# Kernel tuning notes

Measured on AMD Instinct MI355X. Metric: run time of the kernel, lower is better.

Reference implementation:

```python
import jax, jax.numpy as jnp
import numpy as np

G, S, D, H, E = 8, 2048, 1024, 4096, 8  # groups, group_size, d_model, ffn_hidden, experts


def setup_inputs() -> dict:
    key = jax.random.key(0)
    ks = jax.random.split(key, 6)
    s = 0.02
    return {
        "x": jax.random.normal(ks[0], (G, S, D), dtype=jnp.float32),
        "gate_w": jax.random.normal(ks[1], (D, E), dtype=jnp.float32) * s,
        "ew1": jax.random.normal(ks[2], (E, D, H), dtype=jnp.float32) * s,
        "eb1": jnp.zeros((E, H), dtype=jnp.float32),
        "ew2": jax.random.normal(ks[3], (E, H, D), dtype=jnp.float32) * s,
        "eb2": jnp.zeros((E, D), dtype=jnp.float32),
        "sw1": jax.random.normal(ks[4], (D, H), dtype=jnp.float32) * s,
        "sb1": jnp.zeros((H,), dtype=jnp.float32),
        "sw2": jax.random.normal(ks[5], (H, D), dtype=jnp.float32) * s,
        "sb2": jnp.zeros((D,), dtype=jnp.float32),
        "expert_capacity": 2048,
    }


def reference(x, gate_w, ew1, eb1, ew2, eb2, sw1, sb1, sw2, sb2, expert_capacity):
    g, s_, d = x.shape
    e = gate_w.shape[1]
    T = g * s_
    cap = int(expert_capacity)

    # ---- Router (inference path) ----
    router_logits = jnp.einsum('gsd,de->gse', x, gate_w)           # (G,S,E)
    router_probs = jax.nn.softmax(router_logits, axis=-1)
    flat_probs = router_probs.transpose(2, 0, 1).reshape(e, T)      # (E,T)
    pad_w = max(0, cap - T)
    if pad_w > 0:
        flat_probs = jnp.pad(flat_probs, ((0, 0), (0, pad_w)),
                             mode='constant', constant_values=-1e9)
    scores, token_indices = jax.lax.top_k(flat_probs, k=cap)        # (E,C)
    scores = jnp.where(scores > -1e8, scores, 0.0)

    # ---- Routed experts: gather -> grouped FFN -> scale -> scatter-add ----
    x_flat = x.reshape(T, d)                                        # (T,D)
    safe_idx = jnp.clip(token_indices, 0, T - 1)                    # guard padded slots
    toks = x_flat[safe_idx]                                         # (E,C,D)
    h = jax.nn.gelu(jnp.einsum('ecd,edh->ech', toks, ew1) + eb1[:, None, :])
    y = jnp.einsum('ech,ehd->ecd', h, ew2) + eb2[:, None, :]        # (E,C,D)
    y = y * scores[..., None]                                       # zero weight kills padded slots
    routed = jnp.zeros_like(x_flat).at[safe_idx.reshape(-1)].add(y.reshape(-1, d))

    # ---- Shared expert over all tokens ----
    shared = jax.nn.gelu(x_flat @ sw1 + sb1) @ sw2 + sb2            # (T,D)

    return (routed + shared).reshape(g, s_, d)
```

## Files before the change

kernel.cpp:

```cpp
#include <hip/hip_runtime.h>

typedef __bf16 bf16;
typedef __bf16 bf16x8 __attribute__((ext_vector_type(8)));
typedef float f32x4 __attribute__((ext_vector_type(4)));

#define NTOK 16384
#define DMODEL 1024
#define HFFN 4096
#define NEXP 8
#define CAP 2048

#define VMCNT(n) asm volatile("s_waitcnt vmcnt(" #n ")" ::: "memory")
#define LGKM0() do { asm volatile("s_waitcnt lgkmcnt(0)" ::: "memory"); \
                     __builtin_amdgcn_sched_barrier(0); } while (0)
#define BARRIER() __builtin_amdgcn_s_barrier()
#define PRIO1() __builtin_amdgcn_s_setprio(1)
#define PRIO0() __builtin_amdgcn_s_setprio(0)

__device__ __forceinline__ void gload16(const void* g, void* l) {
  __builtin_amdgcn_global_load_lds((const __attribute__((address_space(1))) void*)g,
                                   (__attribute__((address_space(3))) void*)l, 16, 0, 0);
}

__device__ __forceinline__ float gelu_f(float v) {
  float t = v * v;
  float s2 = v * fmaf(0.10294358f, t, 2.3022084f);
  float e = __builtin_exp2f(-s2);
  return v * __builtin_amdgcn_rcpf(1.0f + e);
}

__device__ __forceinline__ void xcd_remap(int& bx, int& by) {
  const int gx = gridDim.x;
  const int lg = 31 - __clz((unsigned)gx);
  const int w = blockIdx.x + gx * blockIdx.y;
  bx = (w >> 3) & (gx - 1);
  by = (w & 7) | (((w >> 3) >> lg) << 3);
}

__global__ __launch_bounds__(256) void cvt_x_kernel(const float* __restrict__ x,
                                                    bf16* __restrict__ xb) {
  int i = blockIdx.x * blockDim.x + threadIdx.x;
  const float4* a = (const float4*)x + (size_t)i * 2;
  float4 v0 = a[0], v1 = a[1];
  bf16x8 o;
  o[0]=(bf16)v0.x; o[1]=(bf16)v0.y; o[2]=(bf16)v0.z; o[3]=(bf16)v0.w;
  o[4]=(bf16)v1.x; o[5]=(bf16)v1.y; o[6]=(bf16)v1.z; o[7]=(bf16)v1.w;
  *(bf16x8*)(xb + (size_t)i * 8) = o;
}

__global__ __launch_bounds__(64) void router_kernel(const float* __restrict__ x,
                                                    const float* __restrict__ gw,
                                                    float* __restrict__ probs) {
  int t = blockIdx.x;
  int l = threadIdx.x;
  int e = l & 7, chunk = l >> 3;
  const float* xr = x + (size_t)t * DMODEL + chunk * 128;
  const float* gwr = gw + (size_t)(chunk * 128) * NEXP + e;
  float a0 = 0.f, a1 = 0.f;
  #pragma unroll
  for (int d = 0; d < 128; d += 8) {
    float4 xv = *(const float4*)(xr + d);
    float4 xw = *(const float4*)(xr + d + 4);
    a0 += xv.x * gwr[(d+0)*8] + xv.y * gwr[(d+1)*8] + xv.z * gwr[(d+2)*8] + xv.w * gwr[(d+3)*8];
    a1 += xw.x * gwr[(d+4)*8] + xw.y * gwr[(d+5)*8] + xw.z * gwr[(d+6)*8] + xw.w * gwr[(d+7)*8];
  }
  float acc = a0 + a1;
  acc += __shfl_xor(acc, 8);
  acc += __shfl_xor(acc, 16);
  acc += __shfl_xor(acc, 32);
  float m = acc;
  m = fmaxf(m, __shfl_xor(m, 1));
  m = fmaxf(m, __shfl_xor(m, 2));
  m = fmaxf(m, __shfl_xor(m, 4));
  float ex = expf(acc - m);
  float s = ex;
  s += __shfl_xor(s, 1); s += __shfl_xor(s, 2); s += __shfl_xor(s, 4);
  if (l < 8) probs[(size_t)e * NTOK + t] = ex / s;
}

__global__ __launch_bounds__(256) void topk_kernel(const float* __restrict__ probs,
                                                   int* __restrict__ oidx,
                                                   float* __restrict__ oscr) {
  const int e = blockIdx.x;
  const float* p = probs + (size_t)e * NTOK;
  const int t = threadIdx.x;
  __shared__ unsigned hist[256];
  __shared__ unsigned sg[256], sq[256];
  __shared__ unsigned bcast[4];
  unsigned pref = 0, krem = CAP;
  for (int pass = 0; pass < 4; ++pass) {
    const int sh = 24 - pass * 8;
    hist[t] = 0;
    __syncthreads();
    for (int j = 0; j < 64; ++j) {
      unsigned u = __float_as_uint(p[t * 64 + j]);
      bool ok = (pass == 0) || ((u >> (sh + 8)) == pref);
      if (ok) atomicAdd(&hist[(u >> sh) & 255u], 1u);
    }
    __syncthreads();
    if (t == 0) {
      unsigned cum = 0; int b = 255;
      for (; b > 0; --b) {
        unsigned c = hist[b];
        if (cum + c >= krem) break;
        cum += c;
      }
      bcast[0] = (pref << 8) | (unsigned)b;
      bcast[1] = krem - cum;
    }
    __syncthreads();
    pref = bcast[0];
    krem = bcast[1];
  }
  const unsigned thr = pref;
  const unsigned neq_take = krem;
  unsigned cgt = 0, ceq = 0;
  for (int j = 0; j < 64; ++j) {
    unsigned u = __float_as_uint(p[t * 64 + j]);
    cgt += (u > thr);
    ceq += (u == thr);
  }
  sg[t] = cgt; sq[t] = ceq;
  __syncthreads();
  if (t == 0) {
    unsigned ag = 0, aq = 0;
    for (int i = 0; i < 256; ++i) {
      unsigned g = sg[i], q = sq[i];
      sg[i] = ag; sq[i] = aq;
      ag += g; aq += q;
    }
    bcast[2] = ag;
  }
  __syncthreads();
  const unsigned ngt = bcast[2];
  unsigned og = sg[t], oq = sq[t];
  int* oi = oidx + e * CAP;
  float* os = oscr + e * CAP;
  for (int j = 0; j < 64; ++j) {
    int tok = t * 64 + j;
    float pv = p[tok];
    unsigned u = __float_as_uint(pv);
    if (u > thr) {
      oi[og] = tok; os[og] = pv; ++og;
    } else if (u == thr) {
      if (oq < neq_take) { oi[ngt + oq] = tok; os[ngt + oq] = pv; }
      ++oq;
    }
  }
}

__global__ __launch_bounds__(256) void transpose_cvt(const float* __restrict__ in_e,
                                                     const float* __restrict__ in_s,
                                                     bf16* __restrict__ outp,
                                                     int R, int C) {
  int z = blockIdx.z;
  const float* in = (z < 8) ? (in_e + (size_t)z * (size_t)R * C) : in_s;
  bf16* out = outp + (size_t)z * (size_t)R * C;
  __shared__ float tile[64][65];
  int tx = threadIdx.x & 63, ty = threadIdx.x >> 6;
  int c0 = blockIdx.x * 64, r0 = blockIdx.y * 64;
  #pragma unroll
  for (int j = 0; j < 16; ++j) {
    int r = ty + j * 4;
    tile[r][tx] = in[(size_t)(r0 + r) * C + c0 + tx];
  }
  __syncthreads();
  #pragma unroll
  for (int j = 0; j < 16; ++j) {
    int c = ty + j * 4;
    out[(size_t)(c0 + c) * R + r0 + tx] = (bf16)tile[tx][c];
  }
}


#define STG_ALO(D, ko) { gload16(srcA0 + (ko), (D) + tid8); gload16(srcA2 + (ko), (D) + 4096 + tid8); }
#define STG_AHI(D, ko) { gload16(srcA1 + (ko), (D) + 8192 + tid8); gload16(srcA3 + (ko), (D) + 12288 + tid8); }
#define STG_BLO(D, ko) { gload16(srcBlo0 + (ko), (D) + 16384 + tid8); gload16(srcBlo1 + (ko), (D) + 20480 + tid8); }
#define STG_BHI(D, ko) { gload16(srcBhi0 + (ko), (D) + 24576 + tid8); gload16(srcBhi1 + (ko), (D) + 28672 + tid8); }

#define RD_A(ARR, D, OFF) \
  _Pragma("unroll") for (int i = 0; i < 4; ++i) { \
    ARR[2*i]   = *(const bf16x8*)((D) + (OFF) + (wr*64 + i*16 + fr)*64 + c0s); \
    ARR[2*i+1] = *(const bf16x8*)((D) + (OFF) + (wr*64 + i*16 + fr)*64 + c1s); \
  }
#define RD_B(ARR, D, OFF) \
  _Pragma("unroll") for (int j = 0; j < 2; ++j) { \
    ARR[2*j]   = *(const bf16x8*)((D) + (OFF) + (wc*32 + j*16 + fr)*64 + c0s); \
    ARR[2*j+1] = *(const bf16x8*)((D) + (OFF) + (wc*32 + j*16 + fr)*64 + c1s); \
  }

#define MFMA_Q(I0, J0, A, B) \
  _Pragma("unroll") for (int i = 0; i < 4; ++i) \
    _Pragma("unroll") for (int j = 0; j < 2; ++j) { \
      acc[(I0)+i][(J0)+j] = __builtin_amdgcn_mfma_f32_16x16x32_bf16((A)[2*i],   (B)[2*j],   acc[(I0)+i][(J0)+j], 0, 0, 0); \
      acc[(I0)+i][(J0)+j] = __builtin_amdgcn_mfma_f32_16x16x32_bf16((A)[2*i+1], (B)[2*j+1], acc[(I0)+i][(J0)+j], 0, 0, 0); \
    }

#define KLOOP(NT) do { \
  bf16* B0_ = smem; \
  bf16* B1_ = smem + 32768; \
   \
  STG_ALO(B0_, 0); STG_BLO(B0_, 0); STG_BHI(B0_, 0); STG_AHI(B0_, 0); \
  STG_ALO(B1_, 64); STG_BLO(B1_, 64); STG_BHI(B1_, 64); \
  VMCNT(6); \
  BARRIER(); \
  RD_A(aA, B0_, 0); RD_B(aB, B0_, 16384); \
  for (int t = 0; t < (NT); t += 2) { \
    const bool st = (t + 2) < (NT); \
    const int ko1 = (t + 1) * 64, ko2 = (t + 2) * 64, ko3 = (t + 3) * 64; \
     \
    LGKM0(); \
    STG_AHI(B1_, ko1); \
    PRIO1(); MFMA_Q(0, 0, aA, aB); PRIO0(); \
    if (st) { VMCNT(10); } else { VMCNT(0); } \
    RD_B(bB, B0_, 24576); \
    BARRIER(); \
     \
    LGKM0(); \
    if (st) STG_ALO(B0_, ko2); \
    PRIO1(); MFMA_Q(0, 2, aA, bB); PRIO0(); \
    if (st) { VMCNT(10); } else { VMCNT(0); } \
    RD_A(aA, B0_, 8192); \
    BARRIER(); \
     \
    LGKM0(); \
    if (st) STG_BLO(B0_, ko2); \
    PRIO1(); MFMA_Q(4, 2, aA, bB); PRIO0(); \
    BARRIER(); \
     \
    LGKM0(); \
    if (st) STG_BHI(B0_, ko2); \
    PRIO1(); MFMA_Q(4, 0, aA, aB); PRIO0(); \
    if (st) { VMCNT(8); } else { VMCNT(0); } \
    RD_A(aA, B1_, 0); RD_B(aB, B1_, 16384); \
    BARRIER(); \
     \
    LGKM0(); \
    if (st) STG_AHI(B0_, ko2); \
    PRIO1(); MFMA_Q(0, 0, aA, aB); PRIO0(); \
    RD_B(bB, B1_, 24576); \
    BARRIER(); \
     \
    LGKM0(); \
    if (st) STG_ALO(B1_, ko3); \
    PRIO1(); MFMA_Q(0, 2, aA, bB); PRIO0(); \
    if (st) { VMCNT(10); } else { VMCNT(0); } \
    RD_A(aA, B1_, 8192); \
    BARRIER(); \
     \
    LGKM0(); \
    if (st) STG_BLO(B1_, ko3); \
    PRIO1(); MFMA_Q(4, 2, aA, bB); PRIO0(); \
    BARRIER(); \
     \
    LGKM0(); \
    if (st) STG_BHI(B1_, ko3); \
    PRIO1(); MFMA_Q(4, 0, aA, aB); PRIO0(); \
    if (st) { VMCNT(10); } else { VMCNT(0); } \
    if (st) { RD_A(aA, B0_, 0); RD_B(aB, B0_, 16384); } \
    BARRIER(); \
  } \
} while (0)

__global__ __launch_bounds__(512, 2) void ffn1_gemm(const bf16* __restrict__ xb,
                                                    const bf16* __restrict__ w1t,
                                                    const float* __restrict__ bias1,
                                                    const int* __restrict__ sel,
                                                    bf16* __restrict__ hout,
                                                    int routed) {
  const int e = blockIdx.z;
  const bf16* Bw = w1t + (routed ? (size_t)e * HFFN * DMODEL : 0);
  const float* bias = bias1 + (routed ? (size_t)e * HFFN : 0);
  bf16* hb = hout + (routed ? (size_t)e * CAP * HFFN : 0);
  int bx, by;
  xcd_remap(bx, by);
  const int m0 = by * 256, n0 = bx * 256;
  __shared__ __align__(16) bf16 smem[65536];
  const int tid = threadIdx.x, lane = tid & 63, wave = tid >> 6;
  const int wr = wave >> 2, wc = wave & 3;
  const int tid8 = tid * 8;

  const int p = tid >> 3, sch = tid & 7;
  const int schs = sch ^ (p & 7);
  const int brow = p + (p & 32);
  const bf16 *srcA0, *srcA1, *srcA2, *srcA3, *srcBlo0, *srcBlo1, *srcBhi0, *srcBhi1;
  {
    int ra0 = routed ? sel[e * CAP + m0 + p]       : (m0 + p);
    int ra1 = routed ? sel[e * CAP + m0 + 64 + p]  : (m0 + 64 + p);
    int ra2 = routed ? sel[e * CAP + m0 + 128 + p] : (m0 + 128 + p);
    int ra3 = routed ? sel[e * CAP + m0 + 192 + p] : (m0 + 192 + p);
    srcA0 = xb + (size_t)ra0 * DMODEL + schs * 8;
    srcA1 = xb + (size_t)ra1 * DMODEL + schs * 8;
    srcA2 = xb + (size_t)ra2 * DMODEL + schs * 8;
    srcA3 = xb + (size_t)ra3 * DMODEL + schs * 8;
    srcBlo0 = Bw + (size_t)(n0 + brow) * DMODEL + schs * 8;
    srcBlo1 = srcBlo0 + (size_t)128 * DMODEL;
    srcBhi0 = srcBlo0 + (size_t)32 * DMODEL;
    srcBhi1 = srcBlo0 + (size_t)160 * DMODEL;
  }

  f32x4 acc[8][4];
  #pragma unroll
  for (int i = 0; i < 8; ++i)
    #pragma unroll
    for (int j = 0; j < 4; ++j) acc[i][j] = (f32x4){0.f, 0.f, 0.f, 0.f};

  const int fr = lane & 15;
  const int k8 = lane >> 4;
  const int sw = lane & 7;
  const int c0s = (k8 ^ sw) * 8;
  const int c1s = ((k8 + 4) ^ sw) * 8;
  bf16x8 aA[8], aB[4], bB[4];

  KLOOP(DMODEL / 64);

  __syncthreads();
  #pragma unroll
  for (int half = 0; half < 2; ++half) {
    if (wr == half) {
      #pragma unroll
      for (int i = 0; i < 8; ++i) {
        #pragma unroll
        for (int j = 0; j < 4; ++j) {
          const int nl = wc * 64 + j * 16 + fr;
          const float bb = bias[n0 + nl];
          #pragma unroll
          for (int q = 0; q < 4; ++q) {
            const int ml = i * 16 + (lane >> 4) * 4 + q;
            smem[ml * 256 + (nl ^ (((ml >> 2) & 7) << 4))] =
                (bf16)gelu_f(acc[i][j][q] + bb);
          }
        }
      }
    }
    __syncthreads();
    #pragma unroll
    for (int pp = 0; pp < 8; ++pp) {
      const int flat = pp * 512 + tid;
      const int row = flat >> 5, nc8 = flat & 31;
      uint4 v = *(const uint4*)(smem + row * 256 + ((nc8 * 8) ^ (((row >> 2) & 7) << 4)));
      *(uint4*)(hb + (size_t)(m0 + half * 128 + row) * HFFN + n0 + nc8 * 8) = v;
    }
    __syncthreads();
  }
}

__global__ __launch_bounds__(512, 2) void ffn2_gemm(const bf16* __restrict__ hbuf,
                                                    const bf16* __restrict__ w2t,
                                                    const float* __restrict__ bias2,
                                                    const int* __restrict__ sel,
                                                    const float* __restrict__ scr,
                                                    float* __restrict__ out,
                                                    int routed) {
  const int e = blockIdx.z;
  const bf16* Ab = hbuf + (routed ? (size_t)e * CAP * HFFN : 0);
  const bf16* Bw = w2t + (routed ? (size_t)e * DMODEL * HFFN : 0);
  const float* bias = bias2 + (routed ? (size_t)e * DMODEL : 0);
  int bx, by;
  xcd_remap(bx, by);
  const int m0 = by * 256, n0 = bx * 256;
  __shared__ __align__(16) bf16 smem[65536];
  __shared__ int s_tok[256];
  __shared__ float s_scl[256];
  const int tid = threadIdx.x, lane = tid & 63, wave = tid >> 6;
  const int wr = wave >> 2, wc = wave & 3;
  const int tid8 = tid * 8;

  const int p = tid >> 3, sch = tid & 7;
  const int schs = sch ^ (p & 7);
  const int brow = p + (p & 32);
  const bf16* srcA0 = Ab + (size_t)(m0 + p) * HFFN + schs * 8;
  const bf16* srcA1 = Ab + (size_t)(m0 + 64 + p) * HFFN + schs * 8;
  const bf16* srcA2 = Ab + (size_t)(m0 + 128 + p) * HFFN + schs * 8;
  const bf16* srcA3 = Ab + (size_t)(m0 + 192 + p) * HFFN + schs * 8;
  const bf16* srcBlo0 = Bw + (size_t)(n0 + brow) * HFFN + schs * 8;
  const bf16* srcBlo1 = srcBlo0 + (size_t)128 * HFFN;
  const bf16* srcBhi0 = srcBlo0 + (size_t)32 * HFFN;
  const bf16* srcBhi1 = srcBlo0 + (size_t)160 * HFFN;
  if (routed && tid < 256) {
    s_tok[tid] = sel[e * CAP + m0 + tid];
    s_scl[tid] = scr[e * CAP + m0 + tid];
  }

  f32x4 acc[8][4];
  #pragma unroll
  for (int i = 0; i < 8; ++i)
    #pragma unroll
    for (int j = 0; j < 4; ++j) acc[i][j] = (f32x4){0.f, 0.f, 0.f, 0.f};

  const int fr = lane & 15;
  const int k8 = lane >> 4;
  const int sw = lane & 7;
  const int c0s = (k8 ^ sw) * 8;
  const int c1s = ((k8 + 4) ^ sw) * 8;
  bf16x8 aA[8], aB[4], bB[4];

  KLOOP(HFFN / 64);

  if (!routed) {
    #pragma unroll
    for (int i = 0; i < 8; ++i) {
      #pragma unroll
      for (int j = 0; j < 4; ++j) {
        const int nl = wc * 64 + j * 16 + fr;
        const float bb = bias[n0 + nl];
        #pragma unroll
        for (int q = 0; q < 4; ++q) {
          const int ml = wr * 128 + i * 16 + (lane >> 4) * 4 + q;
          out[(size_t)(m0 + ml) * DMODEL + n0 + nl] = acc[i][j][q] + bb;
        }
      }
    }
  } else {
    __syncthreads();
    #pragma unroll
    for (int i = 0; i < 8; ++i) {
      #pragma unroll
      for (int j = 0; j < 4; ++j) {
        const int nl = wc * 64 + j * 16 + fr;
        const float bb = bias[n0 + nl];
        #pragma unroll
        for (int q = 0; q < 4; ++q) {
          const int ml = wr * 128 + i * 16 + (lane >> 4) * 4 + q;
          const int tok = s_tok[ml];
          const float sc = s_scl[ml];
          atomicAdd(out + (size_t)tok * DMODEL + n0 + nl, (acc[i][j][q] + bb) * sc);
        }
      }
    }
  }
}

extern "C" void kernel_launch(void* const* d_in, const int* in_sizes, int n_in,
                              void* d_out, int out_size, void* d_ws, size_t ws_size,
                              hipStream_t stream) {
  const float* x   = (const float*)d_in[0];
  const float* gw  = (const float*)d_in[1];
  const float* ew1 = (const float*)d_in[2];
  const float* eb1 = (const float*)d_in[3];
  const float* ew2 = (const float*)d_in[4];
  const float* eb2 = (const float*)d_in[5];
  const float* sw1 = (const float*)d_in[6];
  const float* sb1 = (const float*)d_in[7];
  const float* sw2 = (const float*)d_in[8];
  const float* sb2 = (const float*)d_in[9];
  float* out = (float*)d_out;

  char* ws = (char*)d_ws;
  size_t off = 0;
  bf16* xb      = (bf16*)(ws + off); off += (size_t)NTOK * DMODEL * 2;
  bf16* w1t     = (bf16*)(ws + off); off += (size_t)9 * HFFN * DMODEL * 2;
  bf16* w2t     = (bf16*)(ws + off); off += (size_t)9 * DMODEL * HFFN * 2;
  bf16* hbuf    = (bf16*)(ws + off); off += (size_t)NTOK * HFFN * 2;
  float* probs  = (float*)(ws + off); off += (size_t)NEXP * NTOK * 4;
  int* selidx   = (int*)(ws + off);   off += (size_t)NEXP * CAP * 4;
  float* selscr = (float*)(ws + off); off += (size_t)NEXP * CAP * 4;

  cvt_x_kernel<<<dim3(NTOK * DMODEL / 8 / 256), dim3(256), 0, stream>>>(x, xb);
  router_kernel<<<dim3(NTOK), dim3(64), 0, stream>>>(x, gw, probs);
  topk_kernel<<<dim3(NEXP), dim3(256), 0, stream>>>(probs, selidx, selscr);
  transpose_cvt<<<dim3(HFFN / 64, DMODEL / 64, 9), dim3(256), 0, stream>>>(ew1, sw1, w1t, DMODEL, HFFN);
  transpose_cvt<<<dim3(DMODEL / 64, HFFN / 64, 9), dim3(256), 0, stream>>>(ew2, sw2, w2t, HFFN, DMODEL);

  ffn1_gemm<<<dim3(HFFN / 256, NTOK / 256, 1), dim3(512), 0, stream>>>(
      xb, w1t + (size_t)8 * HFFN * DMODEL, sb1, (const int*)nullptr, hbuf, 0);
  ffn2_gemm<<<dim3(DMODEL / 256, NTOK / 256, 1), dim3(512), 0, stream>>>(
      hbuf, w2t + (size_t)8 * DMODEL * HFFN, sb2, (const int*)nullptr, (const float*)nullptr, out, 0);

  ffn1_gemm<<<dim3(HFFN / 256, CAP / 256, NEXP), dim3(512), 0, stream>>>(
      xb, w1t, eb1, selidx, hbuf, 1);
  ffn2_gemm<<<dim3(DMODEL / 256, CAP / 256, NEXP), dim3(512), 0, stream>>>(
      hbuf, w2t, eb2, selidx, selscr, out, 1);
}
```

Measured before the change: 838.3 us.

## Reschedule GEMM K-loop with two barriers per phase and rotating B fragment registers

Restructures the ping-pong LDS pipeline in the shared KLOOP macro used by both FFN GEMMs. Each MFMA quarter is now bracketed by a barrier before and after, with the LDS fragment reads issued just ahead of it. The B fragments rotate between two register sets (S1/S2), and the prologue now waits for the whole first stage to land instead of a partial vmcnt. The aim is to tighten the order of LDS reads against global-to-LDS staging and keep waves in lockstep. In exchange it doubles the barrier count and may expose more LDS latency before each MFMA group.

```diff
diff --git a/kernel.cpp b/kernel.cpp
--- a/kernel.cpp
+++ b/kernel.cpp
@@ -199,65 +199,61 @@
 #define KLOOP(NT) do { \
   bf16* B0_ = smem; \
   bf16* B1_ = smem + 32768; \
-   \
-  STG_ALO(B0_, 0); STG_BLO(B0_, 0); STG_BHI(B0_, 0); STG_AHI(B0_, 0); \
-  STG_ALO(B1_, 64); STG_BLO(B1_, 64); STG_BHI(B1_, 64); \
-  VMCNT(6); \
+  STG_ALO(B0_, 0); STG_BHI(B0_, 0); STG_AHI(B0_, 0); STG_BLO(B0_, 0); \
+  VMCNT(0); \
   BARRIER(); \
-  RD_A(aA, B0_, 0); RD_B(aB, B0_, 16384); \
+  RD_B(S1, B0_, 16384); \
+  STG_BLO(B1_, 64); STG_ALO(B1_, 64); STG_BHI(B1_, 64); \
   for (int t = 0; t < (NT); t += 2) { \
     const bool st = (t + 2) < (NT); \
-    const int ko1 = (t + 1) * 64, ko2 = (t + 2) * 64, ko3 = (t + 3) * 64; \
-     \
-    LGKM0(); \
+    const int ko1 = (t+1)*64, ko2 = (t+2)*64, ko3 = (t+3)*64; \
+     \
+    RD_A(aA, B0_, 0); \
     STG_AHI(B1_, ko1); \
-    PRIO1(); MFMA_Q(0, 0, aA, aB); PRIO0(); \
-    if (st) { VMCNT(10); } else { VMCNT(0); } \
-    RD_B(bB, B0_, 24576); \
-    BARRIER(); \
-     \
-    LGKM0(); \
+    BARRIER(); LGKM0(); \
+    PRIO1(); MFMA_Q(0,0,aA,S1); PRIO0(); \
+    BARRIER(); \
+     \
+    RD_B(S2, B0_, 24576); \
+    if (st) STG_BLO(B0_, ko2); \
+    BARRIER(); LGKM0(); \
+    PRIO1(); MFMA_Q(0,2,aA,S2); PRIO0(); \
+    BARRIER(); \
+     \
+    RD_A(aA, B0_, 8192); \
     if (st) STG_ALO(B0_, ko2); \
-    PRIO1(); MFMA_Q(0, 2, aA, bB); PRIO0(); \
-    if (st) { VMCNT(10); } else { VMCNT(0); } \
-    RD_A(aA, B0_, 8192); \
-    BARRIER(); \
-     \
-    LGKM0(); \
-    if (st) STG_BLO(B0_, ko2); \
-    PRIO1(); MFMA_Q(4, 2, aA, bB); PRIO0(); \
-    BARRIER(); \
-     \
-    LGKM0(); \
-    if (st) STG_BHI(B0_, ko2); \
-    PRIO1(); MFMA_Q(4, 0, aA, aB); PRIO0(); \
-    if (st) { VMCNT(8); } else { VMCNT(0); } \
-    RD_A(aA, B1_, 0); RD_B(aB, B1_, 16384); \
-    BARRIER(); \
-     \
-    LGKM0(); \
+    BARRIER(); LGKM0(); \
+    PRIO1(); MFMA_Q(4,2,aA,S2); PRIO0(); \
+    BARRIER(); \
+     \
+    if (st) { STG_BHI(B0_, ko2); VMCNT(6); } else { VMCNT(0); } \
+    RD_B(S2, B1_, 16384); \
+    BARRIER(); LGKM0(); \
+    PRIO1(); MFMA_Q(4,0,aA,S1); PRIO0(); \
+    BARRIER(); \
+     \
+    RD_A(aA, B1_, 0); \
     if (st) STG_AHI(B0_, ko2); \
-    PRIO1(); MFMA_Q(0, 0, aA, aB); PRIO0(); \
-    RD_B(bB, B1_, 24576); \
-    BARRIER(); \
-     \
-    LGKM0(); \
+    BARRIER(); LGKM0(); \
+    PRIO1(); MFMA_Q(0,0,aA,S2); PRIO0(); \
+    BARRIER(); \
+     \
+    RD_B(S1, B1_, 24576); \
+    if (st) STG_BLO(B1_, ko3); \
+    BARRIER(); LGKM0(); \
+    PRIO1(); MFMA_Q(0,2,aA,S1); PRIO0(); \
+    BARRIER(); \
+     \
+    RD_A(aA, B1_, 8192); \
     if (st) STG_ALO(B1_, ko3); \
-    PRIO1(); MFMA_Q(0, 2, aA, bB); PRIO0(); \
-    if (st) { VMCNT(10); } else { VMCNT(0); } \
-    RD_A(aA, B1_, 8192); \
-    BARRIER(); \
-     \
-    LGKM0(); \
-    if (st) STG_BLO(B1_, ko3); \
-    PRIO1(); MFMA_Q(4, 2, aA, bB); PRIO0(); \
-    BARRIER(); \
-     \
-    LGKM0(); \
-    if (st) STG_BHI(B1_, ko3); \
-    PRIO1(); MFMA_Q(4, 0, aA, aB); PRIO0(); \
-    if (st) { VMCNT(10); } else { VMCNT(0); } \
-    if (st) { RD_A(aA, B0_, 0); RD_B(aB, B0_, 16384); } \
+    BARRIER(); LGKM0(); \
+    PRIO1(); MFMA_Q(4,2,aA,S1); PRIO0(); \
+    BARRIER(); \
+     \
+    if (st) { STG_BHI(B1_, ko3); VMCNT(6); RD_B(S1, B0_, 16384); } \
+    else { VMCNT(0); } \
+    BARRIER(); LGKM0(); \
+    PRIO1(); MFMA_Q(4,0,aA,S2); PRIO0(); \
     BARRIER(); \
   } \
 } while (0)
@@ -310,7 +306,7 @@
   const int sw = lane & 7;
   const int c0s = (k8 ^ sw) * 8;
   const int c1s = ((k8 + 4) ^ sw) * 8;
-  bf16x8 aA[8], aB[4], bB[4];
+  bf16x8 aA[8], S1[4], S2[4];
 
   KLOOP(DMODEL / 64);
 
@@ -393,7 +389,7 @@
   const int sw = lane & 7;
   const int c0s = (k8 ^ sw) * 8;
   const int c1s = ((k8 + 4) ^ sw) * 8;
-  bf16x8 aA[8], aB[4], bB[4];
+  bf16x8 aA[8], S1[4], S2[4];
 
   KLOOP(HFFN / 64);
 
```

After: 853.7 us. No clear change (+1.8%).
